# Optimization experiments

Hardware: AMD Instinct MI355X
Metric: run time of the kernel (lower is better)

## Reference

```python
import jax, jax.numpy as jnp
import numpy as np

B, DIM, H, W = 8, 384, 64, 64
HEADS = 8
D = DIM // HEADS          # 48
D2 = D // 2               # 24
DU = D // 3 * 2           # 32 (ratio=3)


def setup_inputs() -> dict:
    key = jax.random.key(0)
    ks = jax.random.split(key, 12)
    s = lambda k, shape, scale=0.05: jax.random.normal(k, shape, jnp.float32) * scale
    return {
        "x": jax.random.normal(ks[0], (B, DIM, H, W), jnp.float32),
        "temperature": jnp.ones((HEADS, 1, 1), jnp.float32),
        "w_qkv": s(ks[1], (3 * DIM, DIM)),          # 1x1 conv, no bias
        "w_dw": s(ks[2], (3 * DIM, 1, 3, 3)),       # depthwise 3x3, groups=3*dim
        "w_proj": s(ks[3], (DIM, HEADS)),           # project_out 1x1
        "w_attn_r": s(ks[4], (1, D)),
        "w_v_r": s(ks[5], (D2, D)),
        "w_up1": s(ks[6], (DU, D2)),
        "b_up1": jnp.zeros((DU,), jnp.float32),
        "ln_w": jnp.ones((DU, HEADS, 1), jnp.float32),
        "ln_b": jnp.zeros((DU, HEADS, 1), jnp.float32),
        "w_up2": s(ks[7], (D, DU)),
        "b_up2": jnp.zeros((D,), jnp.float32),
        "w_attn_l": s(ks[8], (D2, D)),
        "w_v_l": s(ks[9], (D2, D)),
    }


def _qkv_attn(x, temperature, w_qkv, w_dw):
    # shared: qkv 1x1 conv -> depthwise 3x3 -> split, normalize, elementwise attn+softmax
    b, c, h, w = x.shape
    qkv = jnp.einsum('bchw,oc->bohw', x, w_qkv)
    qkv = jax.lax.conv_general_dilated(
        qkv, w_dw, (1, 1), 'SAME', feature_group_count=3 * c,
        dimension_numbers=('NCHW', 'OIHW', 'NCHW'))
    q, k, v = jnp.split(qkv, 3, axis=1)
    rs = lambda t: t.reshape(b, HEADS, D, h * w)  # b (head d) h w -> b head d (hw)
    q, k, v = rs(q), rs(k), rs(v)
    qn = q / jnp.maximum(jnp.linalg.norm(q, axis=-1, keepdims=True), 1e-12)
    kn = k / jnp.maximum(jnp.linalg.norm(k, axis=-1, keepdims=True), 1e-12)
    attn = jax.nn.softmax(qn * kn * temperature, axis=-1)  # [b, head, d, s]
    return attn, v


def _forward(x, temperature, w_qkv, w_dw, w_proj, w_attn_r, w_v_r,
             w_up1, b_up1, ln_w, ln_b, w_up2, b_up2, w_attn_l, w_v_l):
    b, c, h, w = x.shape
    attn, v = _qkv_attn(x, temperature, w_qkv, w_dw)

    # ---- spatial_pool (channel gating) ----
    input_x = jnp.einsum('bhds,od->bhos', v, w_v_r)                 # conv_v_right: [b,head,d2,s]
    cm = jax.nn.softmax(jnp.einsum('bhds,d->bhs', attn, w_attn_r[0]), axis=-1)  # conv_attn_right + softmax
    ctx = jnp.einsum('bhs,bhjs->bhj', cm, input_x)                  # [b,head,d2]
    ctx = ctx.transpose(0, 2, 1)[..., None]                         # [b, d2, head, 1]
    u = jnp.einsum('bchl,oc->bohl', ctx, w_up1) + b_up1[None, :, None, None]  # [b, DU, head, 1]
    mu = u.mean(axis=(1, 2, 3), keepdims=True)
    var = u.var(axis=(1, 2, 3), keepdims=True)
    u = (u - mu) / jnp.sqrt(var + 1e-5) * ln_w[None] + ln_b[None]   # LayerNorm([DU, 8, 1])
    u = jax.nn.relu(u)
    u = jnp.einsum('bchl,oc->bohl', u, w_up2) + b_up2[None, :, None, None]    # [b, D, head, 1]
    mask_ch = jax.nn.sigmoid(u).reshape(b, c, 1, 1)                 # view(b, head*D, 1, 1)
    out_channel = x * mask_ch

    # ---- channel_pool (spatial gating) ----
    g = jnp.einsum('bhds,od->bhos', attn, w_attn_l)                 # conv_attn_left: [b,head,d2,s]
    avg = jax.nn.softmax(g.mean(axis=-1), axis=-1)                  # avg-pool over s, softmax over d2
    theta = jnp.einsum('bhds,od->bhos', v, w_v_l)                   # conv_v_left: [b,head,d2,s]
    ctx2 = jnp.einsum('bhd,bhds->bhs', avg, theta)                  # matmul: [b,head,s]
    mask_sp = jax.nn.sigmoid(ctx2).reshape(b, HEADS, h, w)
    mask_sp = jnp.einsum('bchw,oc->bohw', mask_sp, w_proj)          # project_out
    out_spatial = x * mask_sp

    return out_spatial + out_channel


def reference(x, temperature, w_qkv, w_dw, w_proj, w_attn_r, w_v_r,
              w_up1, b_up1, ln_w, ln_b, w_up2, b_up2, w_attn_l, w_v_l):
    return _forward(x, temperature, w_qkv, w_dw, w_proj, w_attn_r, w_v_r,
                    w_up1, b_up1, ln_w, ln_b, w_up2, b_up2, w_attn_l, w_v_l)
```

## Files before the change

### kernel.cpp

```cpp
#include <hip/hip_runtime.h>
#include <math.h>


#define S4096 4096
#define C384  384
#define OC    1152

typedef unsigned short bfraw;
typedef unsigned int   u32;
typedef __attribute__((ext_vector_type(8))) short bf16x8;
typedef __attribute__((ext_vector_type(4))) float f32x4;

typedef __attribute__((address_space(3))) unsigned int lds_u32;
typedef const __attribute__((address_space(1))) unsigned int glb_u32;
__device__ __forceinline__ void gll16(const void* g, void* l) {
    __builtin_amdgcn_global_load_lds((glb_u32*)g, (lds_u32*)l, 16, 0, 0);
}

__device__ __forceinline__ bfraw f2bf(float f) {
    union { float f; u32 u; } c; c.f = f;
    u32 r = c.u + 0x7FFFu + ((c.u >> 16) & 1u);
    return (bfraw)(r >> 16);
}
__device__ __forceinline__ float bf2f(bfraw u) {
    union { u32 u; float f; } c; c.u = ((u32)u) << 16;
    return c.f;
}
__device__ __forceinline__ void unpack8(uint4 v, float* f) {
    f[0] = bf2f((bfraw)(v.x & 0xffff)); f[1] = bf2f((bfraw)(v.x >> 16));
    f[2] = bf2f((bfraw)(v.y & 0xffff)); f[3] = bf2f((bfraw)(v.y >> 16));
    f[4] = bf2f((bfraw)(v.z & 0xffff)); f[5] = bf2f((bfraw)(v.z >> 16));
    f[6] = bf2f((bfraw)(v.w & 0xffff)); f[7] = bf2f((bfraw)(v.w >> 16));
}
__device__ __forceinline__ uint4 pack8(const float* f) {
    union { bfraw us[8]; uint4 q; } p;
    #pragma unroll
    for (int i = 0; i < 8; i++) p.us[i] = f2bf(f[i]);
    return p.q;
}

__device__ __forceinline__ float blk_red(float v, float* s4, bool ismax) {
    #pragma unroll
    for (int off = 32; off; off >>= 1) {
        float o = __shfl_down(v, off, 64);
        v = ismax ? fmaxf(v, o) : (v + o);
    }
    __syncthreads();
    if ((threadIdx.x & 63) == 0) s4[threadIdx.x >> 6] = v;
    __syncthreads();
    return ismax ? fmaxf(fmaxf(s4[0], s4[1]), fmaxf(s4[2], s4[3]))
                 : ((s4[0] + s4[1]) + (s4[2] + s4[3]));
}

__global__ __launch_bounds__(256) void kA_prep(
    const float* __restrict__ w_qkv, bfraw* __restrict__ wF,
    const float* __restrict__ w_attn_l, const float* __restrict__ w_v_l,
    float* __restrict__ weff) {
    if (blockIdx.x == 216) {
        __shared__ float avg[24];
        const int tid = threadIdx.x;
        if (tid < 24) {
            float a = 0.f;
            for (int d = 0; d < 48; d++) a += w_attn_l[tid * 48 + d];
            avg[tid] = a * (1.f / 4096.f);
        }
        __syncthreads();
        if (tid == 0) {
            float M = -3.402823466e+38f;
            for (int o = 0; o < 24; o++) M = fmaxf(M, avg[o]);
            float S = 0.f;
            for (int o = 0; o < 24; o++) { avg[o] = __expf(avg[o] - M); S += avg[o]; }
            float inv = 1.f / S;
            for (int o = 0; o < 24; o++) avg[o] *= inv;
        }
        __syncthreads();
        if (tid < 48) {
            float a = 0.f;
            for (int o = 0; o < 24; o++) a += avg[o] * w_v_l[o * 48 + tid];
            weff[tid] = a;
        }
        return;
    }
    const int id = blockIdx.x * 256 + threadIdx.x;
    const int ob = id / 768, rem = id % 768;
    const int c = rem / 48, kb = rem % 48;
    const float* src = w_qkv + (size_t)(ob * 16 + c) * C384 + kb * 8;
    float f[8];
    *(float4*)f       = *(const float4*)src;
    *(float4*)(f + 4) = *(const float4*)(src + 4);
    *(uint4*)&wF[((size_t)(ob * 48 + kb) * 16 + c) * 8] = pack8(f);
}

__global__ __launch_bounds__(256) void kB_tr(
    const float* __restrict__ x, bfraw* __restrict__ xF, int b0) {
    const int cb = blockIdx.x, sb = blockIdx.y, bl = blockIdx.z;
    const int c0 = cb * 16, s0 = sb * 256;
    const int tid = threadIdx.x;
    __shared__ alignas(16) bfraw lt[16][264];
    {
        const int r = tid >> 4, seg = tid & 15;
        const float* src = x + ((size_t)(b0 + bl) * C384 + c0 + r) * S4096 + s0 + seg * 16;
        float f[16];
        #pragma unroll
        for (int i = 0; i < 4; i++) *(float4*)(f + i * 4) = *(const float4*)(src + i * 4);
        *(uint4*)&lt[r][seg * 16]     = pack8(f);
        *(uint4*)&lt[r][seg * 16 + 8] = pack8(f + 8);
    }
    __syncthreads();
    const int sbl = tid >> 4, c = tid & 15;
    bfraw* xFb = xF + (size_t)bl * S4096 * C384;
    #pragma unroll
    for (int kbl = 0; kbl < 2; kbl++) {
        union { bfraw us[8]; uint4 q; } p;
        #pragma unroll
        for (int j = 0; j < 8; j++) p.us[j] = lt[kbl * 8 + j][sbl * 16 + c];
        const size_t idx = (((size_t)((s0 >> 4) + sbl) * 48) + (c0 >> 3) + kbl) * 128 + c * 8;
        *(uint4*)&xFb[idx] = p.q;
    }
}

__global__ __launch_bounds__(512) void k1_gemm(
    const bfraw* __restrict__ wF, const bfraw* __restrict__ xF,
    bfraw* __restrict__ pre, int b0) {
    __shared__ alignas(16) bfraw b_sm[2][4096];
    const int tid = threadIdx.x;
    const int wave = tid >> 6, lane = tid & 63;
    const int sT = blockIdx.x, oTb = blockIdx.y, bl = blockIdx.z;
    const bfraw* xFb = xF + (size_t)bl * S4096 * C384;

    const int rbs = tid >> 6, ocs = (tid >> 4) & 3, rws = tid & 15;
    const bfraw* pB = xFb + ((size_t)((sT * 8 + rbs) * 48 + ocs) * 16 + rws) * 8;

    const int wo = wave >> 1;
    const int ws_ = wave & 1;
    const int l15 = lane & 15, kq = lane >> 4;

    const bfraw* pA[4];
    bool aval[4];
    #pragma unroll
    for (int m = 0; m < 4; m++) {
        int rbase = oTb * 16 + wo * 4 + m;
        aval[m] = (rbase < 72);
        if (!aval[m]) rbase = 0;
        pA[m] = wF + (((size_t)rbase * 48 + kq) * 16 + l15) * 8;
    }

    f32x4 acc[4][4];
    #pragma unroll
    for (int m = 0; m < 4; m++)
        #pragma unroll
        for (int n = 0; n < 4; n++) acc[m][n] = (f32x4){0, 0, 0, 0};

    gll16(pB, &b_sm[0][(size_t)tid * 8]);
    bf16x8 a_cur[4];
    #pragma unroll
    for (int m = 0; m < 4; m++) a_cur[m] = *(const bf16x8*)(pA[m]);
    __syncthreads();

    #pragma unroll
    for (int ks = 0; ks < 12; ks++) {
        const bfraw* cb = b_sm[ks & 1];
        bf16x8 bq[4];
        #pragma unroll
        for (int n = 0; n < 4; n++)
            bq[n] = *(const bf16x8*)&cb[((ws_ * 4 + n) * 64 + lane) * 8];
        bf16x8 a_nxt[4];
        if (ks < 11) {
            bfraw* nb = (bfraw*)b_sm[(ks & 1) ^ 1];
            gll16(pB + (size_t)(ks + 1) * 512, nb + (size_t)tid * 8);
            #pragma unroll
            for (int m = 0; m < 4; m++)
                a_nxt[m] = *(const bf16x8*)(pA[m] + (size_t)(ks + 1) * 512);
        }
        __builtin_amdgcn_s_setprio(1);
        #pragma unroll
        for (int m = 0; m < 4; m++)
            #pragma unroll
            for (int n = 0; n < 4; n++)
                acc[m][n] = __builtin_amdgcn_mfma_f32_16x16x32_bf16(a_cur[m], bq[n], acc[m][n], 0, 0, 0);
        __builtin_amdgcn_s_setprio(0);
        if (ks < 11) {
            #pragma unroll
            for (int m = 0; m < 4; m++) a_cur[m] = a_nxt[m];
        }
        __syncthreads();
    }

    bfraw* op = pre + (size_t)bl * OC * S4096;
    const int orow0 = oTb * 256 + wo * 64 + (lane >> 4) * 4;
    const int scol0 = sT * 128 + ws_ * 64 + l15;
    #pragma unroll
    for (int m = 0; m < 4; m++) {
        if (!aval[m]) continue;
        #pragma unroll
        for (int n = 0; n < 4; n++)
            #pragma unroll
            for (int r = 0; r < 4; r++)
                op[(size_t)(orow0 + m * 16 + r) * S4096 + scol0 + n * 16] = f2bf(acc[m][n][r]);
    }
}

__device__ __forceinline__ void stencil8(const bfraw* plane, const float* w9,
                                         int ypad, int k7, int x0, float* acc) {
    #pragma unroll
    for (int j = 0; j < 8; j++) acc[j] = 0.f;
    #pragma unroll
    for (int dy = 0; dy < 3; dy++) {
        uint4 rv = *(const uint4*)&plane[(ypad + dy) * 64 + x0];
        float r[8]; unpack8(rv, r);
        float lft = __shfl_up(r[7], 1);
        float rgt = __shfl_down(r[0], 1);
        if (k7 == 0) lft = 0.f;
        if (k7 == 7) rgt = 0.f;
        const float w0 = w9[dy*3], w1 = w9[dy*3+1], w2 = w9[dy*3+2];
        acc[0] += w0*lft + w1*r[0] + w2*r[1];
        #pragma unroll
        for (int j = 1; j < 7; j++) acc[j] += w0*r[j-1] + w1*r[j] + w2*r[j+1];
        acc[7] += w0*r[6] + w1*r[7] + w2*rgt;
    }
}

__global__ __launch_bounds__(256) void k2f(
    const bfraw* __restrict__ pre, const float* __restrict__ w_dw,
    const float* __restrict__ temperature,
    bfraw* __restrict__ av, int b0) {
    const int idx = blockIdx.x;
    const int bl  = blockIdx.y;
    const int h   = idx / 48;
    const int tid = threadIdx.x;
    __shared__ alignas(16) bfraw pl[3][66 * 64];
    __shared__ float s4[4];

    const size_t pbase = (size_t)bl * OC * S4096;
    #pragma unroll
    for (int p = 0; p < 3; p++) {
        const bfraw* src = pre + pbase + (size_t)(idx + p * C384) * S4096;
        uint4 a = *(const uint4*)&src[tid * 16];
        uint4 b = *(const uint4*)&src[tid * 16 + 8];
        int y = tid >> 2, xq = (tid & 3) * 16;
        *(uint4*)&pl[p][(y + 1) * 64 + xq]     = a;
        *(uint4*)&pl[p][(y + 1) * 64 + xq + 8] = b;
    }
    if (tid < 64) {
        #pragma unroll
        for (int p = 0; p < 3; p++) { pl[p][tid] = 0; pl[p][65 * 64 + tid] = 0; }
    }
    float wq[9], wk[9], wv[9];
    #pragma unroll
    for (int i = 0; i < 9; i++) {
        wq[i] = w_dw[idx * 9 + i];
        wk[i] = w_dw[(idx + C384) * 9 + i];
        wv[i] = w_dw[(idx + 768) * 9 + i];
    }
    __syncthreads();

    const int sid0 = tid,        y0 = sid0 >> 3, k70 = sid0 & 7, x00 = k70 * 8;
    const int sid1 = tid + 256,  y1 = sid1 >> 3, k71 = sid1 & 7, x01 = k71 * 8;
    float qo[16], ko[16], vo[16];
    stencil8(pl[0], wq, y0, k70, x00, qo);
    stencil8(pl[0], wq, y1, k71, x01, qo + 8);
    stencil8(pl[1], wk, y0, k70, x00, ko);
    stencil8(pl[1], wk, y1, k71, x01, ko + 8);
    stencil8(pl[2], wv, y0, k70, x00, vo);
    stencil8(pl[2], wv, y1, k71, x01, vo + 8);

    float sq = 0.f, sk = 0.f;
    #pragma unroll
    for (int i = 0; i < 16; i++) { sq += qo[i] * qo[i]; sk += ko[i] * ko[i]; }
    float Sq = blk_red(sq, s4, false);
    float Sk = blk_red(sk, s4, false);
    float scale = temperature[h] /
        (fmaxf(sqrtf(Sq), 1e-12f) * fmaxf(sqrtf(Sk), 1e-12f));
    float lm = -3.402823466e+38f;
    #pragma unroll
    for (int i = 0; i < 16; i++) { qo[i] = qo[i] * ko[i] * scale; lm = fmaxf(lm, qo[i]); }
    float M = blk_red(lm, s4, true);
    float ls = 0.f;
    #pragma unroll
    for (int i = 0; i < 16; i++) { qo[i] = __expf(qo[i] - M); ls += qo[i]; }
    float Z = blk_red(ls, s4, false);
    float invZ = 1.f / Z;
    #pragma unroll
    for (int i = 0; i < 16; i++) qo[i] *= invZ;

    bfraw* adst = av + ((size_t)bl * 768 + idx) * S4096;
    bfraw* vdst = av + ((size_t)bl * 768 + 384 + idx) * S4096;
    *(uint4*)&adst[y0 * 64 + x00] = pack8(qo);
    *(uint4*)&adst[y1 * 64 + x01] = pack8(qo + 8);
    *(uint4*)&vdst[y0 * 64 + x00] = pack8(vo);
    *(uint4*)&vdst[y1 * 64 + x01] = pack8(vo + 8);
}

__global__ __launch_bounds__(256) void k4a(
    const bfraw* __restrict__ av, const float* __restrict__ w_attn_r,
    const float* __restrict__ weff,
    bfraw* __restrict__ cmraw, bfraw* __restrict__ c2raw, int b0) {
    const int h = blockIdx.x, bl = blockIdx.y, st = blockIdx.z;
    const int b = b0 + bl;
    const int tid = threadIdx.x;
    __shared__ float swr[48], swf[48];
    if (tid < 48) { swr[tid] = w_attn_r[tid]; swf[tid] = weff[tid]; }
    __syncthreads();
    const int s_off = st * 1024 + tid * 4;
    const bfraw* abase = av + ((size_t)bl * 768 + h * 48) * S4096 + s_off;
    const bfraw* vbase = abase + (size_t)384 * S4096;
    float cmr[4] = {0,0,0,0}, c2[4] = {0,0,0,0};
    for (int d = 0; d < 48; d++) {
        uint2 ua = *(const uint2*)(abase + (size_t)d * S4096);
        uint2 uv = *(const uint2*)(vbase + (size_t)d * S4096);
        const float wr = swr[d], wf = swf[d];
        cmr[0] += bf2f((bfraw)(ua.x & 0xffff)) * wr;
        cmr[1] += bf2f((bfraw)(ua.x >> 16))    * wr;
        cmr[2] += bf2f((bfraw)(ua.y & 0xffff)) * wr;
        cmr[3] += bf2f((bfraw)(ua.y >> 16))    * wr;
        c2[0]  += bf2f((bfraw)(uv.x & 0xffff)) * wf;
        c2[1]  += bf2f((bfraw)(uv.x >> 16))    * wf;
        c2[2]  += bf2f((bfraw)(uv.y & 0xffff)) * wf;
        c2[3]  += bf2f((bfraw)(uv.y >> 16))    * wf;
    }
    const size_t o = ((size_t)(b * 8 + h)) * S4096 + s_off;
    union { bfraw us[4]; uint2 q; } pa, pb;
    #pragma unroll
    for (int j = 0; j < 4; j++) { pa.us[j] = f2bf(cmr[j]); pb.us[j] = f2bf(c2[j]); }
    *(uint2*)(cmraw + o) = pa.q;
    *(uint2*)(c2raw + o) = pb.q;
}

__global__ __launch_bounds__(256) void k4b(
    const bfraw* __restrict__ cmraw, const bfraw* __restrict__ c2raw,
    bfraw* __restrict__ cmb, bfraw* __restrict__ msp, int b0) {
    const int h = blockIdx.x, bl = blockIdx.y, b = b0 + bl;
    const int tid = threadIdx.x;
    __shared__ float s4[4];
    const size_t base = ((size_t)(b * 8 + h)) * S4096 + tid * 16;
    float v[16];
    { uint4 a = *(const uint4*)(cmraw + base), c = *(const uint4*)(cmraw + base + 8);
      unpack8(a, v); unpack8(c, v + 8); }
    float lm = -3.402823466e+38f;
    #pragma unroll
    for (int i = 0; i < 16; i++) lm = fmaxf(lm, v[i]);
    float M = blk_red(lm, s4, true);
    float ls = 0.f;
    #pragma unroll
    for (int i = 0; i < 16; i++) { v[i] = __expf(v[i] - M); ls += v[i]; }
    float Z = blk_red(ls, s4, false);
    float inv = 1.f / Z;
    #pragma unroll
    for (int i = 0; i < 16; i++) v[i] *= inv;
    *(uint4*)(cmb + base)     = pack8(v);
    *(uint4*)(cmb + base + 8) = pack8(v + 8);
    float sg[16];
    { uint4 a = *(const uint4*)(c2raw + base), c = *(const uint4*)(c2raw + base + 8);
      unpack8(a, sg); unpack8(c, sg + 8); }
    #pragma unroll
    for (int i = 0; i < 16; i++) sg[i] = 1.f / (1.f + __expf(-sg[i]));
    *(uint4*)(msp + base)     = pack8(sg);
    *(uint4*)(msp + base + 8) = pack8(sg + 8);
}

__global__ __launch_bounds__(256) void k5_vc(
    const bfraw* __restrict__ av, const bfraw* __restrict__ cmb,
    float* __restrict__ vc, int b0) {
    const int idx = blockIdx.x;
    const int bl = blockIdx.y, b = b0 + bl;
    const int h = idx / 48;
    const int tid = threadIdx.x;
    const bfraw* vr = av + ((size_t)bl * 768 + 384 + idx) * S4096 + tid * 16;
    const bfraw* cr = cmb + ((size_t)(b * 8 + h)) * S4096 + tid * 16;
    float vv[16], cc[16];
    { uint4 a = *(const uint4*)vr, c = *(const uint4*)(vr + 8); unpack8(a, vv); unpack8(c, vv + 8); }
    { uint4 a = *(const uint4*)cr, c = *(const uint4*)(cr + 8); unpack8(a, cc); unpack8(c, cc + 8); }
    float a = 0.f;
    #pragma unroll
    for (int i = 0; i < 16; i++) a += vv[i] * cc[i];
    __shared__ float s4[4];
    float S = blk_red(a, s4, false);
    if (tid == 0) vc[b * C384 + idx] = S;
}

__global__ __launch_bounds__(256) void k6_gate(
    const float* __restrict__ vc, const float* __restrict__ w_v_r,
    const float* __restrict__ w_up1, const float* __restrict__ b_up1,
    const float* __restrict__ ln_w, const float* __restrict__ ln_b,
    const float* __restrict__ w_up2, const float* __restrict__ b_up2,
    float* __restrict__ mch, int b0) {
    const int b = b0 + blockIdx.x;
    const int tid = threadIdx.x;
    __shared__ float s_vc[384], s_ctx[192], s_u[256], s4[4];
    for (int i = tid; i < 384; i += 256) s_vc[i] = vc[b * C384 + i];
    __syncthreads();
    if (tid < 192) {
        int hh = tid / 24, o = tid % 24;
        float a = 0.f;
        for (int d = 0; d < 48; d++) a += w_v_r[o * 48 + d] * s_vc[hh * 48 + d];
        s_ctx[hh * 24 + o] = a;
    }
    __syncthreads();
    float uval;
    {
        int o = tid >> 3, hh = tid & 7;
        float a = b_up1[o];
        for (int c = 0; c < 24; c++) a += w_up1[o * 24 + c] * s_ctx[hh * 24 + c];
        uval = a;
    }
    float mu  = blk_red(uval, s4, false) * (1.f / 256.f);
    float dv  = uval - mu;
    float var = blk_red(dv * dv, s4, false) * (1.f / 256.f);
    float un  = dv * rsqrtf(var + 1e-5f) * ln_w[tid] + ln_b[tid];
    s_u[tid] = fmaxf(un, 0.f);
    __syncthreads();
    for (int t = tid; t < 384; t += 256) {
        int o2 = t >> 3, hh = t & 7;
        float a = b_up2[o2];
        for (int o = 0; o < 32; o++) a += w_up2[o2 * 32 + o] * s_u[o * 8 + hh];
        mch[b * C384 + t] = 1.f / (1.f + __expf(-a));
    }
}

__global__ __launch_bounds__(256) void k7_out(
    const float* __restrict__ x, const float* __restrict__ w_proj,
    const float* __restrict__ mch, const bfraw* __restrict__ msp,
    float* __restrict__ out, int b0) {
    const int st = blockIdx.x, cg = blockIdx.y, bl = blockIdx.z;
    const int b = b0 + bl;
    const int tid = threadIdx.x;
    const int s0 = st * 256, c0 = cg * 48;
    __shared__ float s_msp[8][256];
    __shared__ float s_mch[48];
    __shared__ float s_wp[48][8];
    for (int i = tid; i < 2048; i += 256) {
        int hh = i >> 8, ss = i & 255;
        s_msp[hh][ss] = bf2f(msp[((size_t)(b * 8 + hh)) * S4096 + s0 + ss]);
    }
    if (tid < 48) s_mch[tid] = mch[b * C384 + c0 + tid];
    for (int i = tid; i < 384; i += 256)
        s_wp[i >> 3][i & 7] = w_proj[(size_t)(c0 + (i >> 3)) * 8 + (i & 7)];
    __syncthreads();

    const int cl = tid >> 6;
    const int s4i = (tid & 63) * 4;
    float4 m[8];
    #pragma unroll
    for (int hh = 0; hh < 8; hh++) m[hh] = *(const float4*)&s_msp[hh][s4i];

    #pragma unroll 4
    for (int j = 0; j < 12; j++) {
        const int cloc = j * 4 + cl;
        const int c = c0 + cloc;
        const float base = s_mch[cloc];
        float4 a = {base, base, base, base};
        #pragma unroll
        for (int hh = 0; hh < 8; hh++) {
            const float wp = s_wp[cloc][hh];
            a.x += wp * m[hh].x; a.y += wp * m[hh].y;
            a.z += wp * m[hh].z; a.w += wp * m[hh].w;
        }
        const size_t o = ((size_t)b * C384 + c) * S4096 + s0 + s4i;
        float4 xv = *(const float4*)(x + o);
        a.x *= xv.x; a.y *= xv.y; a.z *= xv.z; a.w *= xv.w;
        *(float4*)(out + o) = a;
    }
}

extern "C" void kernel_launch(void* const* d_in, const int* in_sizes, int n_in,
                              void* d_out, int out_size, void* d_ws, size_t ws_size,
                              hipStream_t stream) {
    const float* x        = (const float*)d_in[0];
    const float* temp     = (const float*)d_in[1];
    const float* w_qkv    = (const float*)d_in[2];
    const float* w_dw     = (const float*)d_in[3];
    const float* w_proj   = (const float*)d_in[4];
    const float* w_attn_r = (const float*)d_in[5];
    const float* w_v_r    = (const float*)d_in[6];
    const float* w_up1    = (const float*)d_in[7];
    const float* b_up1    = (const float*)d_in[8];
    const float* ln_w     = (const float*)d_in[9];
    const float* ln_b     = (const float*)d_in[10];
    const float* w_up2    = (const float*)d_in[11];
    const float* b_up2    = (const float*)d_in[12];
    const float* w_attn_l = (const float*)d_in[13];
    const float* w_v_l    = (const float*)d_in[14];
    float* out = (float*)d_out;
    char* ws = (char*)d_ws;

    size_t off = 0;
    auto alloc = [&](size_t bytes) {
        size_t o = off; off = (off + bytes + 255) & ~(size_t)255; return o;
    };
    bfraw* cmraw = (bfraw*)(ws + alloc((size_t)64 * S4096 * 2));
    bfraw* c2raw = (bfraw*)(ws + alloc((size_t)64 * S4096 * 2));
    bfraw* cmb   = (bfraw*)(ws + alloc((size_t)64 * S4096 * 2));
    bfraw* msp   = (bfraw*)(ws + alloc((size_t)64 * S4096 * 2));
    float* vc    = (float*)(ws + alloc(3072 * 4));
    float* mch   = (float*)(ws + alloc(3072 * 4));
    float* weff  = (float*)(ws + alloc(256));
    bfraw* wF    = (bfraw*)(ws + alloc((size_t)55296 * 16));
    const size_t big_xF  = (size_t)S4096 * C384 * 2;
    const size_t big_pre = (size_t)OC * S4096 * 2;
    const size_t big_av  = (size_t)768 * S4096 * 2;
    int nb = (ws_size >= off + 8 * (big_xF + big_pre + big_av)) ? 8 : 1;
    bfraw* xF  = (bfraw*)(ws + alloc((size_t)nb * big_xF));
    bfraw* pre = (bfraw*)(ws + alloc((size_t)nb * big_pre));
    bfraw* av  = (bfraw*)(ws + alloc((size_t)nb * big_av));

    kA_prep<<<217, 256, 0, stream>>>(w_qkv, wF, w_attn_l, w_v_l, weff);
    for (int b0 = 0; b0 < 8; b0 += nb) {
        kB_tr<<<dim3(24, 16, nb), 256, 0, stream>>>(x, xF, b0);
        k1_gemm<<<dim3(32, 5, nb), 512, 0, stream>>>(wF, xF, pre, b0);
        k2f<<<dim3(384, nb), 256, 0, stream>>>(pre, w_dw, temp, av, b0);
        k4a<<<dim3(8, nb, 4), 256, 0, stream>>>(av, w_attn_r, weff, cmraw, c2raw, b0);
        k4b<<<dim3(8, nb), 256, 0, stream>>>(cmraw, c2raw, cmb, msp, b0);
        k5_vc<<<dim3(384, nb), 256, 0, stream>>>(av, cmb, vc, b0);
        k6_gate<<<dim3(nb), 256, 0, stream>>>(vc, w_v_r, w_up1, b_up1,
                                              ln_w, ln_b, w_up2, b_up2, mch, b0);
        k7_out<<<dim3(16, 8, nb), 256, 0, stream>>>(x, w_proj, mch, msp, out, b0);
    }
}
```

Measured before the change: 136.5 us.

## Keep full-K activation tile resident in LDS and loop over all output tiles

The QKV GEMM now loads each block's 64-column by 384-K activation tile into LDS once, then iterates over all nine 128-row output tiles, streaming weights from global memory. This replaces the 2D grid of 512-thread blocks that re-read the activation tile for each output-row block and double-buffered K slices with per-step barriers. It removes the redundant activation traffic and the barriers, but leaves only 64×nb blocks of 2 waves each, which lowers occupancy and parallelism and makes each block serialize nine output tiles.

```diff
diff --git a/kernel.cpp b/kernel.cpp
--- a/kernel.cpp
+++ b/kernel.cpp
@@ -119,84 +119,79 @@
     }
 }
 
-__global__ __launch_bounds__(512) void k1_gemm(
+__global__ __launch_bounds__(128) void k1_gemm(
     const bfraw* __restrict__ wF, const bfraw* __restrict__ xF,
     bfraw* __restrict__ pre, int b0) {
-    __shared__ alignas(16) bfraw b_sm[2][4096];
+    __shared__ alignas(16) bfraw b_sm[24576];
     const int tid = threadIdx.x;
     const int wave = tid >> 6, lane = tid & 63;
-    const int sT = blockIdx.x, oTb = blockIdx.y, bl = blockIdx.z;
+    const int sT = blockIdx.x, bl = blockIdx.y;
     const bfraw* xFb = xF + (size_t)bl * S4096 * C384;
-
-    const int rbs = tid >> 6, ocs = (tid >> 4) & 3, rws = tid & 15;
-    const bfraw* pB = xFb + ((size_t)((sT * 8 + rbs) * 48 + ocs) * 16 + rws) * 8;
-
-    const int wo = wave >> 1;
-    const int ws_ = wave & 1;
     const int l15 = lane & 15, kq = lane >> 4;
 
-    const bfraw* pA[4];
-    bool aval[4];
-    #pragma unroll
-    for (int m = 0; m < 4; m++) {
-        int rbase = oTb * 16 + wo * 4 + m;
-        aval[m] = (rbase < 72);
-        if (!aval[m]) rbase = 0;
-        pA[m] = wF + (((size_t)rbase * 48 + kq) * 16 + l15) * 8;
-    }
-
-    f32x4 acc[4][4];
-    #pragma unroll
-    for (int m = 0; m < 4; m++)
-        #pragma unroll
-        for (int n = 0; n < 4; n++) acc[m][n] = (f32x4){0, 0, 0, 0};
-
-    gll16(pB, &b_sm[0][(size_t)tid * 8]);
+    {
+        const bfraw* src0 = xFb + (size_t)sT * 4 * 48 * 128;
+        #pragma unroll
+        for (int r = 0; r < 24; r++)
+            gll16(src0 + (size_t)(tid + r * 128) * 8, &b_sm[(size_t)(tid + r * 128) * 8]);
+    }
+    asm volatile("s_waitcnt vmcnt(0)" ::: "memory");
+    __syncthreads();
+
+    const int rb_w = wave * 4;
+    auto aAddr = [&](int oT, int m, int ks) {
+        return wF + (((size_t)(oT * 8 + rb_w + m) * 48 + ks * 4 + kq) * 16 + l15) * 8;
+    };
+
     bf16x8 a_cur[4];
     #pragma unroll
-    for (int m = 0; m < 4; m++) a_cur[m] = *(const bf16x8*)(pA[m]);
-    __syncthreads();
-
-    #pragma unroll
-    for (int ks = 0; ks < 12; ks++) {
-        const bfraw* cb = b_sm[ks & 1];
-        bf16x8 bq[4];
-        #pragma unroll
-        for (int n = 0; n < 4; n++)
-            bq[n] = *(const bf16x8*)&cb[((ws_ * 4 + n) * 64 + lane) * 8];
-        bf16x8 a_nxt[4];
-        if (ks < 11) {
-            bfraw* nb = (bfraw*)b_sm[(ks & 1) ^ 1];
-            gll16(pB + (size_t)(ks + 1) * 512, nb + (size_t)tid * 8);
+    for (int m = 0; m < 4; m++) a_cur[m] = *(const bf16x8*)aAddr(0, m, 0);
+
+    bfraw* op = pre + (size_t)bl * OC * S4096;
+    const int scol0 = sT * 64 + l15;
+    const int orow_l = (lane >> 4) * 4;
+
+    for (int oT = 0; oT < 9; oT++) {
+        f32x4 acc[4][4];
+        #pragma unroll
+        for (int m = 0; m < 4; m++)
+            #pragma unroll
+            for (int n = 0; n < 4; n++) acc[m][n] = (f32x4){0, 0, 0, 0};
+
+        #pragma unroll
+        for (int ks = 0; ks < 12; ks++) {
+            bf16x8 bq[4];
+            #pragma unroll
+            for (int n = 0; n < 4; n++)
+                bq[n] = *(const bf16x8*)&b_sm[(((size_t)n * 48 + ks * 4 + kq) * 16 + l15) * 8];
+            const bool have = (ks < 11) || (oT < 8);
+            const int noT = (ks < 11) ? oT : oT + 1;
+            const int nks = (ks < 11) ? ks + 1 : 0;
+            bf16x8 a_nxt[4];
+            if (have) {
+                #pragma unroll
+                for (int m = 0; m < 4; m++) a_nxt[m] = *(const bf16x8*)aAddr(noT, m, nks);
+            }
+            __builtin_amdgcn_s_setprio(1);
             #pragma unroll
             for (int m = 0; m < 4; m++)
-                a_nxt[m] = *(const bf16x8*)(pA[m] + (size_t)(ks + 1) * 512);
+                #pragma unroll
+                for (int n = 0; n < 4; n++)
+                    acc[m][n] = __builtin_amdgcn_mfma_f32_16x16x32_bf16(a_cur[m], bq[n], acc[m][n], 0, 0, 0);
+            __builtin_amdgcn_s_setprio(0);
+            if (have) {
+                #pragma unroll
+                for (int m = 0; m < 4; m++) a_cur[m] = a_nxt[m];
+            }
         }
-        __builtin_amdgcn_s_setprio(1);
+        const int orow0 = oT * 128 + wave * 64 + orow_l;
         #pragma unroll
         for (int m = 0; m < 4; m++)
             #pragma unroll
             for (int n = 0; n < 4; n++)
-                acc[m][n] = __builtin_amdgcn_mfma_f32_16x16x32_bf16(a_cur[m], bq[n], acc[m][n], 0, 0, 0);
-        __builtin_amdgcn_s_setprio(0);
-        if (ks < 11) {
-            #pragma unroll
-            for (int m = 0; m < 4; m++) a_cur[m] = a_nxt[m];
-        }
-        __syncthreads();
-    }
-
-    bfraw* op = pre + (size_t)bl * OC * S4096;
-    const int orow0 = oTb * 256 + wo * 64 + (lane >> 4) * 4;
-    const int scol0 = sT * 128 + ws_ * 64 + l15;
-    #pragma unroll
-    for (int m = 0; m < 4; m++) {
-        if (!aval[m]) continue;
-        #pragma unroll
-        for (int n = 0; n < 4; n++)
-            #pragma unroll
-            for (int r = 0; r < 4; r++)
-                op[(size_t)(orow0 + m * 16 + r) * S4096 + scol0 + n * 16] = f2bf(acc[m][n][r]);
+                #pragma unroll
+                for (int r = 0; r < 4; r++)
+                    op[(size_t)(orow0 + m * 16 + r) * S4096 + scol0 + n * 16] = f2bf(acc[m][n][r]);
     }
 }
 
@@ -506,7 +501,7 @@
     kA_prep<<<217, 256, 0, stream>>>(w_qkv, wF, w_attn_l, w_v_l, weff);
     for (int b0 = 0; b0 < 8; b0 += nb) {
         kB_tr<<<dim3(24, 16, nb), 256, 0, stream>>>(x, xF, b0);
-        k1_gemm<<<dim3(32, 5, nb), 512, 0, stream>>>(wF, xF, pre, b0);
+        k1_gemm<<<dim3(64, nb), 128, 0, stream>>>(wF, xF, pre, b0);
         k2f<<<dim3(384, nb), 256, 0, stream>>>(pre, w_dw, temp, av, b0);
         k4a<<<dim3(8, nb, 4), 256, 0, stream>>>(av, w_attn_r, weff, cmraw, c2raw, b0);
         k4b<<<dim3(8, nb), 256, 0, stream>>>(cmraw, c2raw, cmb, msp, b0);
```

Result: faster. 129.2 us (-5.4%).

## Drop LDS staging in QKV GEMM; load both operands directly into registers

Applied to the files above, without the earlier changes.

The QKV 1x1-conv GEMM no longer stages the activation tile in LDS with global_load_lds and barriers. Each wave now loads both weight and activation fragments straight from global memory into registers and double-buffers them, using 256-thread blocks on a 16x18 grid with 64x256 output tiles. This removes LDS traffic, the per-step barriers and the padded, masked output rows. In exchange there is no cross-wave sharing of the B tile, so global and L2 load traffic goes up.

```diff
diff --git a/kernel.cpp b/kernel.cpp
--- a/kernel.cpp
+++ b/kernel.cpp
@@ -10,12 +10,6 @@
 typedef unsigned int   u32;
 typedef __attribute__((ext_vector_type(8))) short bf16x8;
 typedef __attribute__((ext_vector_type(4))) float f32x4;
-
-typedef __attribute__((address_space(3))) unsigned int lds_u32;
-typedef const __attribute__((address_space(1))) unsigned int glb_u32;
-__device__ __forceinline__ void gll16(const void* g, void* l) {
-    __builtin_amdgcn_global_load_lds((glb_u32*)g, (lds_u32*)l, 16, 0, 0);
-}
 
 __device__ __forceinline__ bfraw f2bf(float f) {
     union { float f; u32 u; } c; c.f = f;
@@ -119,30 +113,24 @@
     }
 }
 
-__global__ __launch_bounds__(512) void k1_gemm(
+__global__ __launch_bounds__(256) void k1_gemm(
     const bfraw* __restrict__ wF, const bfraw* __restrict__ xF,
     bfraw* __restrict__ pre, int b0) {
-    __shared__ alignas(16) bfraw b_sm[2][4096];
     const int tid = threadIdx.x;
     const int wave = tid >> 6, lane = tid & 63;
-    const int sT = blockIdx.x, oTb = blockIdx.y, bl = blockIdx.z;
+    const int sG = blockIdx.x, oT = blockIdx.y, bl = blockIdx.z;
     const bfraw* xFb = xF + (size_t)bl * S4096 * C384;
-
-    const int rbs = tid >> 6, ocs = (tid >> 4) & 3, rws = tid & 15;
-    const bfraw* pB = xFb + ((size_t)((sT * 8 + rbs) * 48 + ocs) * 16 + rws) * 8;
-
-    const int wo = wave >> 1;
-    const int ws_ = wave & 1;
     const int l15 = lane & 15, kq = lane >> 4;
 
+    const int rbase = oT * 4;
+    const int cbase = (sG * 4 + wave) * 4;
+
     const bfraw* pA[4];
-    bool aval[4];
-    #pragma unroll
-    for (int m = 0; m < 4; m++) {
-        int rbase = oTb * 16 + wo * 4 + m;
-        aval[m] = (rbase < 72);
-        if (!aval[m]) rbase = 0;
-        pA[m] = wF + (((size_t)rbase * 48 + kq) * 16 + l15) * 8;
+    const bfraw* pB[4];
+    #pragma unroll
+    for (int i = 0; i < 4; i++) {
+        pA[i] = wF  + (((size_t)(rbase + i) * 48 + kq) * 16 + l15) * 8;
+        pB[i] = xFb + (((size_t)(cbase + i) * 48 + kq) * 16 + l15) * 8;
     }
 
     f32x4 acc[4][4];
@@ -151,53 +139,44 @@
         #pragma unroll
         for (int n = 0; n < 4; n++) acc[m][n] = (f32x4){0, 0, 0, 0};
 
-    gll16(pB, &b_sm[0][(size_t)tid * 8]);
-    bf16x8 a_cur[4];
-    #pragma unroll
-    for (int m = 0; m < 4; m++) a_cur[m] = *(const bf16x8*)(pA[m]);
-    __syncthreads();
+    bf16x8 a_cur[4], b_cur[4];
+    #pragma unroll
+    for (int i = 0; i < 4; i++) {
+        a_cur[i] = *(const bf16x8*)(pA[i]);
+        b_cur[i] = *(const bf16x8*)(pB[i]);
+    }
 
     #pragma unroll
     for (int ks = 0; ks < 12; ks++) {
-        const bfraw* cb = b_sm[ks & 1];
-        bf16x8 bq[4];
-        #pragma unroll
-        for (int n = 0; n < 4; n++)
-            bq[n] = *(const bf16x8*)&cb[((ws_ * 4 + n) * 64 + lane) * 8];
-        bf16x8 a_nxt[4];
+        bf16x8 a_nxt[4], b_nxt[4];
         if (ks < 11) {
-            bfraw* nb = (bfraw*)b_sm[(ks & 1) ^ 1];
-            gll16(pB + (size_t)(ks + 1) * 512, nb + (size_t)tid * 8);
             #pragma unroll
-            for (int m = 0; m < 4; m++)
-                a_nxt[m] = *(const bf16x8*)(pA[m] + (size_t)(ks + 1) * 512);
-        }
-        __builtin_amdgcn_s_setprio(1);
+            for (int i = 0; i < 4; i++) {
+                a_nxt[i] = *(const bf16x8*)(pA[i] + (size_t)(ks + 1) * 512);
+                b_nxt[i] = *(const bf16x8*)(pB[i] + (size_t)(ks + 1) * 512);
+            }
+        }
         #pragma unroll
         for (int m = 0; m < 4; m++)
             #pragma unroll
             for (int n = 0; n < 4; n++)
-                acc[m][n] = __builtin_amdgcn_mfma_f32_16x16x32_bf16(a_cur[m], bq[n], acc[m][n], 0, 0, 0);
-        __builtin_amdgcn_s_setprio(0);
+                acc[m][n] = __builtin_amdgcn_mfma_f32_16x16x32_bf16(a_cur[m], b_cur[n], acc[m][n], 0, 0, 0);
         if (ks < 11) {
             #pragma unroll
-            for (int m = 0; m < 4; m++) a_cur[m] = a_nxt[m];
-        }
-        __syncthreads();
+            for (int i = 0; i < 4; i++) { a_cur[i] = a_nxt[i]; b_cur[i] = b_nxt[i]; }
+        }
     }
 
     bfraw* op = pre + (size_t)bl * OC * S4096;
-    const int orow0 = oTb * 256 + wo * 64 + (lane >> 4) * 4;
-    const int scol0 = sT * 128 + ws_ * 64 + l15;
-    #pragma unroll
-    for (int m = 0; m < 4; m++) {
-        if (!aval[m]) continue;
+    const int orow0 = oT * 64 + (lane >> 4) * 4;
+    const int scol0 = (sG * 4 + wave) * 64 + l15;
+    #pragma unroll
+    for (int m = 0; m < 4; m++)
         #pragma unroll
         for (int n = 0; n < 4; n++)
             #pragma unroll
             for (int r = 0; r < 4; r++)
                 op[(size_t)(orow0 + m * 16 + r) * S4096 + scol0 + n * 16] = f2bf(acc[m][n][r]);
-    }
 }
 
 __device__ __forceinline__ void stencil8(const bfraw* plane, const float* w9,
@@ -506,7 +485,7 @@
     kA_prep<<<217, 256, 0, stream>>>(w_qkv, wF, w_attn_l, w_v_l, weff);
     for (int b0 = 0; b0 < 8; b0 += nb) {
         kB_tr<<<dim3(24, 16, nb), 256, 0, stream>>>(x, xF, b0);
-        k1_gemm<<<dim3(32, 5, nb), 512, 0, stream>>>(wF, xF, pre, b0);
+        k1_gemm<<<dim3(16, 18, nb), 256, 0, stream>>>(wF, xF, pre, b0);
         k2f<<<dim3(384, nb), 256, 0, stream>>>(pre, w_dw, temp, av, b0);
         k4a<<<dim3(8, nb, 4), 256, 0, stream>>>(av, w_attn_r, weff, cmraw, c2raw, b0);
         k4b<<<dim3(8, nb), 256, 0, stream>>>(cmraw, c2raw, cmb, msp, b0);
```

After: 130.5 us. -4.4%, faster.
